# Kernel tuning notes

Measured on AMD Instinct MI355X. Metric: run time of the kernel, lower is better.

## Reference

```python
import jax, jax.numpy as jnp
import numpy as np

N_NODES = 100000
N_EDGES = 1600000
D_IN = 128
D_OUT = 128
LN_EPS = 1e-5
MEAN_EPS = 1e-8


def setup_inputs() -> dict:
    key = jax.random.key(0)
    ks = jax.random.split(key, 8)
    x = jax.random.normal(ks[0], (N_NODES, D_IN), dtype=jnp.float32)
    edge_index = jax.random.randint(ks[1], (2, N_EDGES), 0, N_NODES, dtype=jnp.int64)
    s = 1.0 / np.sqrt(D_IN)
    W_agg = jax.random.uniform(ks[2], (D_OUT, D_IN), jnp.float32, -s, s)
    b_agg = jax.random.uniform(ks[3], (D_OUT,), jnp.float32, -s, s)
    W_self = jax.random.uniform(ks[4], (D_OUT, D_IN), jnp.float32, -s, s)
    b_self = jax.random.uniform(ks[5], (D_OUT,), jnp.float32, -s, s)
    gamma = jnp.ones((D_OUT,), jnp.float32)
    beta = jnp.zeros((D_OUT,), jnp.float32)
    return {"x": x, "edge_index": edge_index, "W_agg": W_agg, "b_agg": b_agg,
            "W_self": W_self, "b_self": b_self, "gamma": gamma, "beta": beta}


def reference(x, edge_index, W_agg, b_agg, W_self, b_self, gamma, beta):
    row, col = edge_index[0], edge_index[1]
    num_nodes = x.shape[0]
    # self path: Linear(in, out)
    self_out = x @ W_self.T + b_self                              # [N, D_OUT]
    # mean aggregation: fused gather + segment-sum (no index_add buffer passes)
    neighbor_sum = jax.ops.segment_sum(x[col], row, num_segments=num_nodes)   # [N, D_IN]
    ones = jnp.ones((col.shape[0], 1), dtype=x.dtype)
    neighbor_count = jax.ops.segment_sum(ones, row, num_segments=num_nodes)   # [N, 1]
    neighbor_mean = neighbor_sum / (neighbor_count + MEAN_EPS)
    agg_out = neighbor_mean @ W_agg.T + b_agg                     # [N, D_OUT]
    # relu -> LayerNorm (dropout is identity at eval)
    h = jax.nn.relu(self_out + agg_out)
    mu = jnp.mean(h, axis=-1, keepdims=True)
    var = jnp.mean(jnp.square(h - mu), axis=-1, keepdims=True)
    return (h - mu) * jax.lax.rsqrt(var + LN_EPS) * gamma + beta
```

## Files before the change

### kernel.cpp

```cpp
#include <hip/hip_runtime.h>

#define N_NODES 100000
#define N_EDGES 1600000
#define D 128
#define RPB 64
#define NBUCKET 1563
#define NBLK 196
#define EPB 8192
#define AGG_CAP 2048
#define XCB 3125
#define SCAN_PAD 1792

constexpr float LN_EPS   = 1e-5f;
constexpr float MEAN_EPS = 1e-8f;

typedef __attribute__((ext_vector_type(8))) short bf16x8;
typedef __attribute__((ext_vector_type(4))) float f32x4;
typedef __attribute__((ext_vector_type(2))) float f32x2;
typedef __attribute__((ext_vector_type(4))) unsigned uint4e;
typedef __attribute__((ext_vector_type(2))) unsigned uint2e;

__device__ inline unsigned short f2bf(float f) {
  union { float f; unsigned u; } v; v.f = f;
  return (unsigned short)((v.u + 0x7FFFu + ((v.u >> 16) & 1u)) >> 16);
}
__device__ inline unsigned pack2(float a, float b) {
  return (unsigned)f2bf(a) | ((unsigned)f2bf(b) << 16);
}

__global__ __launch_bounds__(256) void prep_sort(
    const float* __restrict__ x, const int* __restrict__ ei,
    const float* __restrict__ Wself, const float* __restrict__ Wagg,
    const float* __restrict__ bself, const float* __restrict__ bagg,
    unsigned char* __restrict__ x8,
    unsigned short* __restrict__ wcat, float* __restrict__ bsum,
    unsigned* __restrict__ ent_sorted, int* __restrict__ chunkoff) {
  __shared__ int ent_s[EPB];
  __shared__ int cnt_s[SCAN_PAD];
  __shared__ int off_s[SCAN_PAD];
  __shared__ int sb[256];
  const int bid = blockIdx.x;
  const int t = threadIdx.x;

  if (bid < NBLK) {
    const int ebase = bid * EPB;
    const int nch = min(EPB, N_EDGES - ebase);
    const int base4 = bid * (EPB / 4);
    const int end4 = base4 + (nch >> 2);

    for (int i = t; i < SCAN_PAD; i += 256) cnt_s[i] = 0;
    __syncthreads();

#pragma unroll
    for (int k = 0; k < EPB / 1024; ++k) {
      int i4 = base4 + k * 256 + t;
      if (i4 < end4) {
        int4 r = ((const int4*)ei)[i4];
        atomicAdd(&cnt_s[r.x >> 6], 1);
        atomicAdd(&cnt_s[r.y >> 6], 1);
        atomicAdd(&cnt_s[r.z >> 6], 1);
        atomicAdd(&cnt_s[r.w >> 6], 1);
      }
    }
    __syncthreads();

    int psum = 0;
#pragma unroll
    for (int i = 0; i < 7; ++i) psum += cnt_s[t * 7 + i];
    sb[t] = psum;
    __syncthreads();
    for (int off = 1; off < 256; off <<= 1) {
      int u = (t >= off) ? sb[t - off] : 0;
      __syncthreads();
      sb[t] += u;
      __syncthreads();
    }
    int run = sb[t] - psum;
#pragma unroll
    for (int i = 0; i < 7; ++i) {
      off_s[t * 7 + i] = run;
      run += cnt_s[t * 7 + i];
    }
    __syncthreads();

    for (int b = t; b < NBUCKET; b += 256)
      chunkoff[b * NBLK + bid] = off_s[b] | (cnt_s[b] << 14);
    __syncthreads();

#pragma unroll
    for (int k = 0; k < EPB / 1024; ++k) {
      int i4 = base4 + k * 256 + t;
      if (i4 < end4) {
        int4 r = ((const int4*)ei)[i4];
        int4 c = ((const int4*)(ei + N_EDGES))[i4];
        int p0 = atomicAdd(&off_s[r.x >> 6], 1);
        ent_s[p0] = ((r.x & 63) << 17) | c.x;
        int p1 = atomicAdd(&off_s[r.y >> 6], 1);
        ent_s[p1] = ((r.y & 63) << 17) | c.y;
        int p2 = atomicAdd(&off_s[r.z >> 6], 1);
        ent_s[p2] = ((r.z & 63) << 17) | c.z;
        int p3 = atomicAdd(&off_s[r.w >> 6], 1);
        ent_s[p3] = ((r.w & 63) << 17) | c.w;
      }
    }
    __syncthreads();

    for (int i = t; i < nch; i += 256)
      ent_sorted[ebase + i] = (unsigned)ent_s[i];
  } else if (bid < NBLK + XCB) {
    const int f = (bid - NBLK) * 4096 + t * 16;
    const float4 v0 = ((const float4*)x)[(f >> 2) + 0];
    const float4 v1 = ((const float4*)x)[(f >> 2) + 1];
    const float4 v2 = ((const float4*)x)[(f >> 2) + 2];
    const float4 v3 = ((const float4*)x)[(f >> 2) + 3];
    unsigned q0 = 0, q1 = 0, q2 = 0, q3 = 0;
    q0 = __builtin_amdgcn_cvt_pk_fp8_f32(v0.x, v0.y, q0, false);
    q0 = __builtin_amdgcn_cvt_pk_fp8_f32(v0.z, v0.w, q0, true);
    q1 = __builtin_amdgcn_cvt_pk_fp8_f32(v1.x, v1.y, q1, false);
    q1 = __builtin_amdgcn_cvt_pk_fp8_f32(v1.z, v1.w, q1, true);
    q2 = __builtin_amdgcn_cvt_pk_fp8_f32(v2.x, v2.y, q2, false);
    q2 = __builtin_amdgcn_cvt_pk_fp8_f32(v2.z, v2.w, q2, true);
    q3 = __builtin_amdgcn_cvt_pk_fp8_f32(v3.x, v3.y, q3, false);
    q3 = __builtin_amdgcn_cvt_pk_fp8_f32(v3.z, v3.w, q3, true);
    uint4e q; q.x = q0; q.y = q1; q.z = q2; q.w = q3;
    *(uint4e*)(x8 + f) = q;
  } else {
    const int blk = bid - NBLK - XCB;
#pragma unroll
    for (int k = 0; k < 8; ++k) {
      int idx = blk * 2048 + k * 256 + t;
      int o = idx >> 8, kc = idx & 255;
      float v = (kc < 128) ? Wself[o * 128 + kc] : Wagg[o * 128 + (kc - 128)];
      wcat[o * 256 + kc] = f2bf(v);
    }
    if (blk == 0 && t < 128) bsum[t] = bself[t] + bagg[t];
    if (blk == 0 && t < 32)
      *(unsigned*)(x8 + (size_t)N_NODES * 128 + t * 4) = 0u;
  }
}

__global__ __launch_bounds__(512, 6) void aggregate(
    const unsigned char* __restrict__ x8, const unsigned* __restrict__ ent_sorted,
    const int* __restrict__ chunkoff, float* out) {
  __shared__ int ent_s[AGG_CAP];
  __shared__ int col_s[AGG_CAP];
  __shared__ int cnt_s[RPB];
  __shared__ int off_s[RPB];
  __shared__ int cur_s[RPB];
  __shared__ int wsum[4];

  const int b = blockIdx.x;
  const int t = threadIdx.x;
  const int w = t >> 6, lane = t & 63;

  int beg = 0, len = 0;
  if (t < NBLK) {
    int pk = chunkoff[b * NBLK + t];
    beg = pk & 16383;
    len = pk >> 14;
  }
  int v = len;
#pragma unroll
  for (int off = 1; off < 64; off <<= 1) {
    int u = __shfl_up(v, off, 64);
    if (lane >= off) v += u;
  }
  if (w < 4 && lane == 63) wsum[w] = v;
  if (t < RPB) cnt_s[t] = 0;
  __syncthreads();
  int n = wsum[0] + wsum[1] + wsum[2] + wsum[3];
  if (n > AGG_CAP) n = AGG_CAP;
  if (t < NBLK) {
    int pre = 0;
    for (int i = 0; i < w; ++i) pre += wsum[i];
    int dst = pre + v - len;
    const unsigned* src = ent_sorted + t * EPB + beg;
    for (int i = 0; i < len; ++i)
      if (dst + i < AGG_CAP) ent_s[dst + i] = (int)src[i];
  }
  __syncthreads();

  for (int i = t; i < n; i += 512) atomicAdd(&cnt_s[ent_s[i] >> 17], 1);
  __syncthreads();

  if (t < RPB) {
    int c = cnt_s[t];
    int sv = c;
#pragma unroll
    for (int off = 1; off < 64; off <<= 1) {
      int u = __shfl_up(sv, off, 64);
      if (t >= off) sv += u;
    }
    off_s[t] = sv - c;
    cur_s[t] = sv - c;
  }
  __syncthreads();

  for (int i = t; i < n; i += 512) {
    int e = ent_s[i];
    int pos = atomicAdd(&cur_s[e >> 17], 1);
    col_s[pos] = e & 0x1FFFF;
  }
  __syncthreads();

  const int e4 = lane >> 4, lq = lane & 15;
  const unsigned co = (unsigned)(lq * 8);
  const int nodebase = b << 6;
  for (int lr = w; lr < RPB; lr += 8) {
    int node = nodebase + lr;
    if (node >= N_NODES) break;
    int rbeg = off_s[lr];
    int deg = cnt_s[lr];
    f32x2 a0 = {0.f, 0.f}, a1 = {0.f, 0.f}, a2 = {0.f, 0.f}, a3 = {0.f, 0.f};
    int j0 = 0;
    for (; j0 + 16 <= deg; j0 += 16) {
      uint2e p[4];
#pragma unroll
      for (int u = 0; u < 4; ++u) {
        int col = col_s[rbeg + j0 + u * 4 + e4];
        p[u] = *(const uint2e*)(x8 + (((unsigned)col << 7) + co));
      }
#pragma unroll
      for (int u = 0; u < 4; ++u) {
        a0 += __builtin_amdgcn_cvt_pk_f32_fp8(p[u].x, false);
        a1 += __builtin_amdgcn_cvt_pk_f32_fp8(p[u].x, true);
        a2 += __builtin_amdgcn_cvt_pk_f32_fp8(p[u].y, false);
        a3 += __builtin_amdgcn_cvt_pk_f32_fp8(p[u].y, true);
      }
    }
    if (j0 < deg) {
      uint2e p[4];
#pragma unroll
      for (int u = 0; u < 4; ++u) {
        int idx = j0 + u * 4 + e4;
        int col = col_s[(rbeg + idx) & (AGG_CAP - 1)];
        col = (idx < deg) ? col : N_NODES;
        p[u] = *(const uint2e*)(x8 + (((unsigned)col << 7) + co));
      }
#pragma unroll
      for (int u = 0; u < 4; ++u) {
        a0 += __builtin_amdgcn_cvt_pk_f32_fp8(p[u].x, false);
        a1 += __builtin_amdgcn_cvt_pk_f32_fp8(p[u].x, true);
        a2 += __builtin_amdgcn_cvt_pk_f32_fp8(p[u].y, false);
        a3 += __builtin_amdgcn_cvt_pk_f32_fp8(p[u].y, true);
      }
    }
    float r0 = a0.x, r1 = a0.y, r2 = a1.x, r3 = a1.y;
    float r4 = a2.x, r5 = a2.y, r6 = a3.x, r7 = a3.y;
    r0 += __shfl_xor(r0, 16, 64); r0 += __shfl_xor(r0, 32, 64);
    r1 += __shfl_xor(r1, 16, 64); r1 += __shfl_xor(r1, 32, 64);
    r2 += __shfl_xor(r2, 16, 64); r2 += __shfl_xor(r2, 32, 64);
    r3 += __shfl_xor(r3, 16, 64); r3 += __shfl_xor(r3, 32, 64);
    r4 += __shfl_xor(r4, 16, 64); r4 += __shfl_xor(r4, 32, 64);
    r5 += __shfl_xor(r5, 16, 64); r5 += __shfl_xor(r5, 32, 64);
    r6 += __shfl_xor(r6, 16, 64); r6 += __shfl_xor(r6, 32, 64);
    r7 += __shfl_xor(r7, 16, 64); r7 += __shfl_xor(r7, 32, 64);
    if (lane < 16) {
      float inv = 1.0f / ((float)deg + MEAN_EPS);
      uint4e o;
      o.x = pack2(r0 * inv, r1 * inv);
      o.y = pack2(r2 * inv, r3 * inv);
      o.z = pack2(r4 * inv, r5 * inv);
      o.w = pack2(r6 * inv, r7 * inv);
      *(uint4e*)((unsigned short*)(out + (size_t)node * D) + lq * 8) = o;
    }
  }
}

__global__ __launch_bounds__(512, 4) void gemm_mfma_ln(
    const float* __restrict__ x, const float* out_mean,
    const unsigned short* __restrict__ wcat, const float* __restrict__ bsum,
    const float* __restrict__ gamma, const float* __restrict__ beta,
    float* out) {
  __shared__ unsigned short Bs[128 * 264];
  __shared__ float bias_s[128];

  const int t = threadIdx.x;
  const int w = t >> 6, lane = t & 63;
  const int q = lane >> 4, s = lane & 15;
  const int base = blockIdx.x * 128;

  if (t < 128) bias_s[t] = bsum[t];

#pragma unroll
  for (int r = 0; r < 8; ++r) {
    int f = r * 512 + t;
    int row = f >> 5, c = f & 31;
    uint4 v = *(const uint4*)(wcat + row * 256 + c * 8);
    *(uint4*)(Bs + row * 264 + c * 8) = v;
  }

  const int arow = base + w * 16 + s;
  const int asafe = (arow < N_NODES) ? arow : 0;
  const float* xrow = x + (size_t)asafe * 128;
  const unsigned short* mrow = (const unsigned short*)(out_mean + (size_t)asafe * 128);
  bf16x8 a[8];
#pragma unroll
  for (int kk = 0; kk < 4; ++kk) {
    const float4 f0 = *(const float4*)(xrow + kk * 32 + q * 8);
    const float4 f1 = *(const float4*)(xrow + kk * 32 + q * 8 + 4);
    bf16x8 av;
    av[0] = (short)f2bf(f0.x); av[1] = (short)f2bf(f0.y);
    av[2] = (short)f2bf(f0.z); av[3] = (short)f2bf(f0.w);
    av[4] = (short)f2bf(f1.x); av[5] = (short)f2bf(f1.y);
    av[6] = (short)f2bf(f1.z); av[7] = (short)f2bf(f1.w);
    a[kk] = av;
  }
#pragma unroll
  for (int kk = 0; kk < 4; ++kk)
    a[4 + kk] = *(const bf16x8*)(mrow + kk * 32 + q * 8);

  __syncthreads();

  f32x4 acc[8];
#pragma unroll
  for (int j = 0; j < 8; ++j) acc[j] = (f32x4)(0.0f);

#pragma unroll
  for (int kk = 0; kk < 8; ++kk) {
    const int ko = kk * 32 + q * 8;
#pragma unroll
    for (int j = 0; j < 8; ++j) {
      bf16x8 bv = *(const bf16x8*)(Bs + (j * 16 + s) * 264 + ko);
      acc[j] = __builtin_amdgcn_mfma_f32_16x16x32_bf16(a[kk], bv, acc[j], 0, 0, 0);
    }
  }

#pragma unroll
  for (int j = 0; j < 8; ++j) {
    float bb = bias_s[j * 16 + s];
#pragma unroll
    for (int r = 0; r < 4; ++r)
      acc[j][r] = fmaxf(acc[j][r] + bb, 0.0f);
  }

  float g[8], be[8];
#pragma unroll
  for (int j = 0; j < 8; ++j) {
    g[j]  = gamma[j * 16 + s];
    be[j] = beta[j * 16 + s];
  }

#pragma unroll
  for (int r = 0; r < 4; ++r) {
    float s1 = 0.f, s2 = 0.f;
#pragma unroll
    for (int j = 0; j < 8; ++j) {
      float h = acc[j][r];
      s1 += h; s2 += h * h;
    }
#pragma unroll
    for (int m = 1; m < 16; m <<= 1) {
      s1 += __shfl_xor(s1, m, 64);
      s2 += __shfl_xor(s2, m, 64);
    }
    int node = base + w * 16 + q * 4 + r;
    if (node < N_NODES) {
      float mu = s1 * (1.0f / 128.0f);
      float var = s2 * (1.0f / 128.0f) - mu * mu;
      float rstd = rsqrtf(var + LN_EPS);
      float* orow = out + (size_t)node * 128;
#pragma unroll
      for (int j = 0; j < 8; ++j)
        orow[j * 16 + s] = (acc[j][r] - mu) * rstd * g[j] + be[j];
    }
  }
}

extern "C" void kernel_launch(void* const* d_in, const int* in_sizes, int n_in,
                              void* d_out, int out_size, void* d_ws, size_t ws_size,
                              hipStream_t stream) {
  const float* x     = (const float*)d_in[0];
  const int*   ei    = (const int*)d_in[1];
  const float* Wagg  = (const float*)d_in[2];
  const float* bagg  = (const float*)d_in[3];
  const float* Wself = (const float*)d_in[4];
  const float* bself = (const float*)d_in[5];
  const float* gamma = (const float*)d_in[6];
  const float* beta  = (const float*)d_in[7];
  float* out = (float*)d_out;

  unsigned char*  x8   = (unsigned char*)d_ws;
  unsigned short* wcat = (unsigned short*)(x8 + (size_t)(N_NODES + 1) * D);
  float* bsum      = (float*)(wcat + 128 * 256);
  unsigned* ent_sorted = (unsigned*)(bsum + 128);
  int* chunkoff    = (int*)(ent_sorted + (size_t)NBLK * EPB);

  prep_sort<<<NBLK + XCB + 16, 256, 0, stream>>>(
      x, ei, Wself, Wagg, bself, bagg, x8, wcat, bsum, ent_sorted, chunkoff);

  aggregate<<<NBUCKET, 512, 0, stream>>>(x8, ent_sorted, chunkoff, out);

  gemm_mfma_ln<<<(N_NODES + 127) / 128, 512, 0, stream>>>(
      x, out, wcat, bsum, gamma, beta, out);
}
```

Before: 196.7 us.

## Fuse neighbor aggregation into MFMA GEMM+LayerNorm kernel via shared-memory means

Merges the aggregate kernel and the GEMM/LayerNorm kernel into one. Each block now handles two 64-node buckets (128 nodes), keeps the bf16 neighbor means in LDS instead of writing them to global memory, and reuses one LDS buffer for both the edge staging and the weight halves. The GEMM is split into two K=128 passes (self weights, then aggregation weights) so the smaller buffer fits. This removes a kernel launch and the global round-trip of the mean tensor, at the cost of higher LDS use per block, fewer blocks, and extra barriers between the two passes.

```diff
diff --git a/kernel.cpp b/kernel.cpp
--- a/kernel.cpp
+++ b/kernel.cpp
@@ -3,11 +3,11 @@
 #define N_NODES 100000
 #define N_EDGES 1600000
 #define D 128
-#define RPB 64
 #define NBUCKET 1563
 #define NBLK 196
 #define EPB 8192
-#define AGG_CAP 2048
+#define CAP2 4096
+#define RPB2 128
 #define XCB 3125
 #define SCAN_PAD 1792
 
@@ -139,25 +139,40 @@
   }
 }
 
-__global__ __launch_bounds__(512, 6) void aggregate(
+__global__ __launch_bounds__(512, 4) void agg_gemm_ln(
     const unsigned char* __restrict__ x8, const unsigned* __restrict__ ent_sorted,
-    const int* __restrict__ chunkoff, float* out) {
-  __shared__ int ent_s[AGG_CAP];
-  __shared__ int col_s[AGG_CAP];
-  __shared__ int cnt_s[RPB];
-  __shared__ int off_s[RPB];
-  __shared__ int cur_s[RPB];
-  __shared__ int wsum[4];
-
-  const int b = blockIdx.x;
+    const int* __restrict__ chunkoff, const float* __restrict__ x,
+    const unsigned short* __restrict__ wcat, const float* __restrict__ bsum,
+    const float* __restrict__ gamma, const float* __restrict__ beta,
+    float* __restrict__ out) {
+  __shared__ __align__(16) unsigned char shbuf[128 * 132 * 2];
+  __shared__ unsigned short mean_s[128 * 132];
+  __shared__ float bias_s[128];
+  __shared__ int cnt_s[RPB2];
+  __shared__ int off_s[RPB2];
+  __shared__ int cur_s[RPB2];
+  __shared__ int wsum[8];
+  __shared__ int rtot;
+
+  int* ent_s = (int*)shbuf;
+  int* col_s = ent_s + CAP2;
+  unsigned short* Bsh = (unsigned short*)shbuf;
+
+  const int bid = blockIdx.x;
   const int t = threadIdx.x;
   const int w = t >> 6, lane = t & 63;
 
+  int sidx = -1, bsel = 0;
+  if (t < NBLK) { sidx = t; bsel = 0; }
+  else if (t >= 256 && t < 256 + NBLK) { sidx = t - 256; bsel = 1; }
   int beg = 0, len = 0;
-  if (t < NBLK) {
-    int pk = chunkoff[b * NBLK + t];
-    beg = pk & 16383;
-    len = pk >> 14;
+  {
+    int brow = 2 * bid + bsel;
+    if (sidx >= 0 && brow < NBUCKET) {
+      int pk = chunkoff[brow * NBLK + sidx];
+      beg = pk & 16383;
+      len = pk >> 14;
+    }
   }
   int v = len;
 #pragma unroll
@@ -165,48 +180,60 @@
     int u = __shfl_up(v, off, 64);
     if (lane >= off) v += u;
   }
-  if (w < 4 && lane == 63) wsum[w] = v;
-  if (t < RPB) cnt_s[t] = 0;
-  __syncthreads();
-  int n = wsum[0] + wsum[1] + wsum[2] + wsum[3];
-  if (n > AGG_CAP) n = AGG_CAP;
-  if (t < NBLK) {
-    int pre = 0;
-    for (int i = 0; i < w; ++i) pre += wsum[i];
+  if (lane == 63) wsum[w] = v;
+  if (t < RPB2) cnt_s[t] = 0;
+  __syncthreads();
+  const int n0raw = wsum[0] + wsum[1] + wsum[2] + wsum[3];
+  int n = n0raw + wsum[4] + wsum[5] + wsum[6] + wsum[7];
+  if (n > CAP2) n = CAP2;
+  if (sidx >= 0 && len > 0) {
+    int pre = bsel ? n0raw : 0;
+    for (int i = (bsel ? 4 : 0); i < w; ++i) pre += wsum[i];
     int dst = pre + v - len;
-    const unsigned* src = ent_sorted + t * EPB + beg;
+    const unsigned* src = ent_sorted + sidx * EPB + beg;
     for (int i = 0; i < len; ++i)
-      if (dst + i < AGG_CAP) ent_s[dst + i] = (int)src[i];
-  }
-  __syncthreads();
-
-  for (int i = t; i < n; i += 512) atomicAdd(&cnt_s[ent_s[i] >> 17], 1);
-  __syncthreads();
-
-  if (t < RPB) {
-    int c = cnt_s[t];
-    int sv = c;
+      if (dst + i < CAP2) ent_s[dst + i] = (int)src[i];
+  }
+  __syncthreads();
+
+  for (int i = t; i < n; i += 512) {
+    int e = ent_s[i];
+    int row = ((e >> 17) & 63) | ((i >= n0raw) ? 64 : 0);
+    atomicAdd(&cnt_s[row], 1);
+  }
+  __syncthreads();
+
+  int c = 0, sv = 0;
+  if (t < RPB2) {
+    c = cnt_s[t];
+    sv = c;
 #pragma unroll
     for (int off = 1; off < 64; off <<= 1) {
       int u = __shfl_up(sv, off, 64);
-      if (t >= off) sv += u;
-    }
-    off_s[t] = sv - c;
-    cur_s[t] = sv - c;
+      if (lane >= off) sv += u;
+    }
+  }
+  if (t == 63) rtot = sv;
+  __syncthreads();
+  if (t < RPB2) {
+    int basec = (t >= 64) ? rtot : 0;
+    off_s[t] = basec + sv - c;
+    cur_s[t] = basec + sv - c;
   }
   __syncthreads();
 
   for (int i = t; i < n; i += 512) {
     int e = ent_s[i];
-    int pos = atomicAdd(&cur_s[e >> 17], 1);
+    int row = ((e >> 17) & 63) | ((i >= n0raw) ? 64 : 0);
+    int pos = atomicAdd(&cur_s[row], 1);
     col_s[pos] = e & 0x1FFFF;
   }
   __syncthreads();
 
   const int e4 = lane >> 4, lq = lane & 15;
   const unsigned co = (unsigned)(lq * 8);
-  const int nodebase = b << 6;
-  for (int lr = w; lr < RPB; lr += 8) {
+  const int nodebase = bid << 7;
+  for (int lr = w; lr < RPB2; lr += 8) {
     int node = nodebase + lr;
     if (node >= N_NODES) break;
     int rbeg = off_s[lr];
@@ -233,7 +260,7 @@
 #pragma unroll
       for (int u = 0; u < 4; ++u) {
         int idx = j0 + u * 4 + e4;
-        int col = col_s[(rbeg + idx) & (AGG_CAP - 1)];
+        int col = col_s[(rbeg + idx) & (CAP2 - 1)];
         col = (idx < deg) ? col : N_NODES;
         p[u] = *(const uint2e*)(x8 + (((unsigned)col << 7) + co));
       }
@@ -262,39 +289,26 @@
       o.y = pack2(r2 * inv, r3 * inv);
       o.z = pack2(r4 * inv, r5 * inv);
       o.w = pack2(r6 * inv, r7 * inv);
-      *(uint4e*)((unsigned short*)(out + (size_t)node * D) + lq * 8) = o;
-    }
-  }
-}
-
-__global__ __launch_bounds__(512, 4) void gemm_mfma_ln(
-    const float* __restrict__ x, const float* out_mean,
-    const unsigned short* __restrict__ wcat, const float* __restrict__ bsum,
-    const float* __restrict__ gamma, const float* __restrict__ beta,
-    float* out) {
-  __shared__ unsigned short Bs[128 * 264];
-  __shared__ float bias_s[128];
-
-  const int t = threadIdx.x;
-  const int w = t >> 6, lane = t & 63;
+      *(uint4e*)(mean_s + lr * 132 + lq * 8) = o;
+    }
+  }
+  if (t < 128) bias_s[t] = bsum[t];
+  __syncthreads();
+
   const int q = lane >> 4, s = lane & 15;
-  const int base = blockIdx.x * 128;
-
-  if (t < 128) bias_s[t] = bsum[t];
-
-#pragma unroll
-  for (int r = 0; r < 8; ++r) {
-    int f = r * 512 + t;
-    int row = f >> 5, c = f & 31;
-    uint4 v = *(const uint4*)(wcat + row * 256 + c * 8);
-    *(uint4*)(Bs + row * 264 + c * 8) = v;
-  }
-
+  const int base = bid << 7;
   const int arow = base + w * 16 + s;
   const int asafe = (arow < N_NODES) ? arow : 0;
   const float* xrow = x + (size_t)asafe * 128;
-  const unsigned short* mrow = (const unsigned short*)(out_mean + (size_t)asafe * 128);
-  bf16x8 a[8];
+
+#pragma unroll
+  for (int r = 0; r < 4; ++r) {
+    int f = r * 512 + t;
+    int row = f >> 4, cc = f & 15;
+    uint4 bv = *(const uint4*)(wcat + row * 256 + cc * 8);
+    *(uint4*)(Bsh + row * 132 + cc * 8) = bv;
+  }
+  bf16x8 a[4];
 #pragma unroll
   for (int kk = 0; kk < 4; ++kk) {
     const float4 f0 = *(const float4*)(xrow + kk * 32 + q * 8);
@@ -306,22 +320,41 @@
     av[6] = (short)f2bf(f1.z); av[7] = (short)f2bf(f1.w);
     a[kk] = av;
   }
+  __syncthreads();
+
+  f32x4 acc[8];
+#pragma unroll
+  for (int j = 0; j < 8; ++j) acc[j] = (f32x4)(0.0f);
+
+#pragma unroll
+  for (int kk = 0; kk < 4; ++kk) {
+    const int ko = kk * 32 + q * 8;
+#pragma unroll
+    for (int j = 0; j < 8; ++j) {
+      bf16x8 bv = *(const bf16x8*)(Bsh + (j * 16 + s) * 132 + ko);
+      acc[j] = __builtin_amdgcn_mfma_f32_16x16x32_bf16(a[kk], bv, acc[j], 0, 0, 0);
+    }
+  }
+  __syncthreads();
+
+#pragma unroll
+  for (int r = 0; r < 4; ++r) {
+    int f = r * 512 + t;
+    int row = f >> 4, cc = f & 15;
+    uint4 bv = *(const uint4*)(wcat + row * 256 + 128 + cc * 8);
+    *(uint4*)(Bsh + row * 132 + cc * 8) = bv;
+  }
 #pragma unroll
   for (int kk = 0; kk < 4; ++kk)
-    a[4 + kk] = *(const bf16x8*)(mrow + kk * 32 + q * 8);
-
-  __syncthreads();
-
-  f32x4 acc[8];
-#pragma unroll
-  for (int j = 0; j < 8; ++j) acc[j] = (f32x4)(0.0f);
-
-#pragma unroll
-  for (int kk = 0; kk < 8; ++kk) {
+    a[kk] = *(const bf16x8*)(mean_s + (w * 16 + s) * 132 + kk * 32 + q * 8);
+  __syncthreads();
+
+#pragma unroll
+  for (int kk = 0; kk < 4; ++kk) {
     const int ko = kk * 32 + q * 8;
 #pragma unroll
     for (int j = 0; j < 8; ++j) {
-      bf16x8 bv = *(const bf16x8*)(Bs + (j * 16 + s) * 264 + ko);
+      bf16x8 bv = *(const bf16x8*)(Bsh + (j * 16 + s) * 132 + ko);
       acc[j] = __builtin_amdgcn_mfma_f32_16x16x32_bf16(a[kk], bv, acc[j], 0, 0, 0);
     }
   }
@@ -389,8 +422,6 @@
   prep_sort<<<NBLK + XCB + 16, 256, 0, stream>>>(
       x, ei, Wself, Wagg, bself, bagg, x8, wcat, bsum, ent_sorted, chunkoff);
 
-  aggregate<<<NBUCKET, 512, 0, stream>>>(x8, ent_sorted, chunkoff, out);
-
-  gemm_mfma_ln<<<(N_NODES + 127) / 128, 512, 0, stream>>>(
-      x, out, wcat, bsum, gamma, beta, out);
+  agg_gemm_ln<<<(NBUCKET + 1) / 2, 512, 0, stream>>>(
+      x8, ent_sorted, chunkoff, x, wcat, bsum, gamma, beta, out);
 }
```

Result: slower. 254.7 us (+29.5%).

## Split GEMM weight staging into two K-halves to halve LDS and raise occupancy

Applied to the files above, without the earlier changes.

The fused GEMM+LayerNorm kernel now stages only half of the concatenated weight matrix in shared memory at a time (128x132 instead of 128x264). It processes the self path (x) first, then reloads the aggregation half of the weights and processes the neighbor-mean half, and it keeps only 4 A fragments live instead of 8. Launch bounds are raised to 8 blocks per CU so that the smaller LDS and register footprint allows more concurrent blocks. The cost is extra barriers and a second serialized weight load per block.

```diff
diff --git a/kernel.cpp b/kernel.cpp
--- a/kernel.cpp
+++ b/kernel.cpp
@@ -267,12 +267,12 @@
   }
 }
 
-__global__ __launch_bounds__(512, 4) void gemm_mfma_ln(
+__global__ __launch_bounds__(512, 8) void gemm_mfma_ln(
     const float* __restrict__ x, const float* out_mean,
     const unsigned short* __restrict__ wcat, const float* __restrict__ bsum,
     const float* __restrict__ gamma, const float* __restrict__ beta,
     float* out) {
-  __shared__ unsigned short Bs[128 * 264];
+  __shared__ unsigned short Bsh[128 * 132];
   __shared__ float bias_s[128];
 
   const int t = threadIdx.x;
@@ -283,18 +283,19 @@
   if (t < 128) bias_s[t] = bsum[t];
 
 #pragma unroll
-  for (int r = 0; r < 8; ++r) {
+  for (int r = 0; r < 4; ++r) {
     int f = r * 512 + t;
-    int row = f >> 5, c = f & 31;
-    uint4 v = *(const uint4*)(wcat + row * 256 + c * 8);
-    *(uint4*)(Bs + row * 264 + c * 8) = v;
+    int row = f >> 4, cc = f & 15;
+    uint4 bv = *(const uint4*)(wcat + row * 256 + cc * 8);
+    *(uint4*)(Bsh + row * 132 + cc * 8) = bv;
   }
 
   const int arow = base + w * 16 + s;
   const int asafe = (arow < N_NODES) ? arow : 0;
   const float* xrow = x + (size_t)asafe * 128;
   const unsigned short* mrow = (const unsigned short*)(out_mean + (size_t)asafe * 128);
-  bf16x8 a[8];
+
+  bf16x8 a[4];
 #pragma unroll
   for (int kk = 0; kk < 4; ++kk) {
     const float4 f0 = *(const float4*)(xrow + kk * 32 + q * 8);
@@ -306,22 +307,41 @@
     av[6] = (short)f2bf(f1.z); av[7] = (short)f2bf(f1.w);
     a[kk] = av;
   }
+  __syncthreads();
+
+  f32x4 acc[8];
+#pragma unroll
+  for (int j = 0; j < 8; ++j) acc[j] = (f32x4)(0.0f);
+
+#pragma unroll
+  for (int kk = 0; kk < 4; ++kk) {
+    const int ko = kk * 32 + q * 8;
+#pragma unroll
+    for (int j = 0; j < 8; ++j) {
+      bf16x8 bv = *(const bf16x8*)(Bsh + (j * 16 + s) * 132 + ko);
+      acc[j] = __builtin_amdgcn_mfma_f32_16x16x32_bf16(a[kk], bv, acc[j], 0, 0, 0);
+    }
+  }
+  __syncthreads();
+
+#pragma unroll
+  for (int r = 0; r < 4; ++r) {
+    int f = r * 512 + t;
+    int row = f >> 4, cc = f & 15;
+    uint4 bv = *(const uint4*)(wcat + row * 256 + 128 + cc * 8);
+    *(uint4*)(Bsh + row * 132 + cc * 8) = bv;
+  }
 #pragma unroll
   for (int kk = 0; kk < 4; ++kk)
-    a[4 + kk] = *(const bf16x8*)(mrow + kk * 32 + q * 8);
-
-  __syncthreads();
-
-  f32x4 acc[8];
-#pragma unroll
-  for (int j = 0; j < 8; ++j) acc[j] = (f32x4)(0.0f);
-
-#pragma unroll
-  for (int kk = 0; kk < 8; ++kk) {
+    a[kk] = *(const bf16x8*)(mrow + kk * 32 + q * 8);
+  __syncthreads();
+
+#pragma unroll
+  for (int kk = 0; kk < 4; ++kk) {
     const int ko = kk * 32 + q * 8;
 #pragma unroll
     for (int j = 0; j < 8; ++j) {
-      bf16x8 bv = *(const bf16x8*)(Bs + (j * 16 + s) * 264 + ko);
+      bf16x8 bv = *(const bf16x8*)(Bsh + (j * 16 + s) * 132 + ko);
       acc[j] = __builtin_amdgcn_mfma_f32_16x16x32_bf16(a[kk], bv, acc[j], 0, 0, 0);
     }
   }
```

Result: slower. 219.1 us (+11.4%).
